# Kernel optimization log

Measured on AMD Instinct MI355X. Metric: run time of the kernel, lower is better.

## Reference

```python
import jax, jax.numpy as jnp
import numpy as np
import math

TOTAL_HEADS = 16
CONTEXTUAL_HEADS = 4


def _compute_slopes(heads):
    def slopes_power_of_2(n):
        start = 2 ** (-2 ** (-(math.log2(n) - 3)))
        ratio = start
        return [start * ratio ** i for i in range(n)]
    if math.log2(heads).is_integer():
        return slopes_power_of_2(heads)
    closest = 2 ** math.floor(math.log2(heads))
    return slopes_power_of_2(closest) + slopes_power_of_2(2 * closest)[0::2][: heads - closest]


def setup_inputs() -> dict:
    key = jax.random.key(0)
    kq, kk = jax.random.split(key)
    b, h, s, d = 1, 16, 2048, 64
    q = jax.random.normal(kq, (b, h, s, d), dtype=jnp.float32)
    k = jax.random.normal(kk, (b, h, s, d), dtype=jnp.float32)
    cross_attn_bias = jnp.zeros((TOTAL_HEADS, 1, 1), dtype=jnp.float32)
    return {"q": q, "k": k, "cross_attn_bias": cross_attn_bias,
            "i": s, "j": s, "offset": 0, "prefix": 16}


def reference(q, k, cross_attn_bias, i, j, offset, prefix):
    b = q.shape[0]
    ch = CONTEXTUAL_HEADS
    slopes = jnp.asarray(_compute_slopes(TOTAL_HEADS), dtype=jnp.float32).reshape(-1, 1, 1)  # [H,1,1]

    # base distance bias: -|j - i|, shape [i, j]
    i_arange = jnp.arange(offset, i + offset)
    j_arange = jnp.arange(j)
    bias = -jnp.abs(j_arange[None, :] - i_arange[:, None]).astype(jnp.float32)

    # contextual heads: data-dependent bias with bidirectional cumsum
    qc = q[:, :ch]
    kc = k[:, :ch]
    dots = jnp.einsum('bhid,bhjd->bhij', qc, kc) * (qc.shape[-1] ** -0.5)
    c_bias = -jax.nn.sigmoid(dots)  # [b, ch, i, j]
    upper = jnp.triu(jnp.ones((i, j), dtype=bool), offset + 1)
    lower = jnp.tril(jnp.ones((i, j), dtype=bool), offset - 1)
    c_up = jnp.cumsum(jnp.where(upper, c_bias, 0.0), axis=-1)
    c_lo = jnp.flip(jnp.cumsum(jnp.flip(jnp.where(lower, c_bias, 0.0), axis=-1), axis=-1), axis=-1)
    c_pos = c_up + c_lo  # [b, ch, i, j]

    bias_full = jnp.concatenate(
        [c_pos, jnp.broadcast_to(bias, (b, TOTAL_HEADS - ch, i, j))], axis=1)  # [b, H, i, j]

    attn_bias = slopes * bias_full  # symmetric path

    # prefix cross-attention bias
    is_prefix = jnp.arange(j) < prefix
    is_cross = (is_prefix[:, None] ^ is_prefix[None, :])[offset:]  # [i, j]
    attn_bias = jnp.where(is_cross, cross_attn_bias, attn_bias)
    return attn_bias
```

## Files before the change

kernel.cpp:

```cpp
#include <hip/hip_runtime.h>
#include <hip/hip_bf16.h>

typedef __bf16 bf16_t;
typedef bf16_t bf16x8 __attribute__((ext_vector_type(8)));
typedef float f32x4 __attribute__((ext_vector_type(4)));

#define TH 16
#define CH 4
#define DD 64
#define SJ 2048
#define SP (SJ + 4)
#define CTXB (SJ/16)
#define NCTX (CH*CTXB)
#define AROWS 32
#define NALIBI ((TH-CH)*(SJ/AROWS))
#define NBLK (NCTX + NALIBI)
#define WSK_BYTES ((size_t)CH*CTXB*2*64*16)

__device__ __forceinline__ float sigmoidf_(float x) {
    return __builtin_amdgcn_rcpf(1.0f + __expf(-x));
}

__device__ __forceinline__ float bsel(unsigned long long u, int e) {
    return __uint_as_float((((unsigned int)(u >> (16 * e)) & 0xffffu) << 16));
}

__global__ __launch_bounds__(256) void prep_kernel(
    const float* __restrict__ k, bf16_t* __restrict__ wsk)
{
    const int t    = (int)blockIdx.x * 256 + (int)threadIdx.x;
    const int h    = t >> 14;
    const int ct   = (t >> 7) & 127;
    const int kk   = (t >> 6) & 1;
    const int lane = t & 63;
    const int col  = ct * 16 + (lane & 15);
    const int db   = kk * 32 + (lane >> 4) * 8;
    const float* p = k + ((size_t)h * SJ + col) * DD + db;
    f32x4 v0 = *(const f32x4*)p;
    f32x4 v1 = *(const f32x4*)(p + 4);
    bf16x8 o;
    #pragma unroll
    for (int e = 0; e < 4; ++e) { o[e] = (bf16_t)v0[e]; o[e + 4] = (bf16_t)v1[e]; }
    *(bf16x8*)(wsk + (size_t)t * 8) = o;
}

__global__ __launch_bounds__(512, 4) void fused_kernel(
    const float* __restrict__ q, const float* __restrict__ k,
    const bf16_t* __restrict__ wsk, int use_ws,
    const float* __restrict__ cab, const int* __restrict__ offp,
    const int* __restrict__ prep, float* __restrict__ out)
{
    __shared__ bf16_t Smb[16][SP];
    __shared__ float tot[16][8];
    __shared__ float pd_in[16], pd_ex[16];
    const int tid  = (int)threadIdx.x;
    const int lane = tid & 63;
    const int w    = tid >> 6;
    const int offset = offp[0];
    const int prefix = prep[0];
    const int bx = (int)blockIdx.x;
    const int m5 = bx % 5;

    if (m5 < 2) {
        const int id = (bx / 5) * 2 + m5;
        const int h  = id >> 7;
        const int r0 = (id & (CTXB - 1)) << 4;
        const float* qh = q + (size_t)h * SJ * DD;
        const float* kh = k + (size_t)h * SJ * DD;

        bf16x8 afrag[2];
        {
            const int row   = r0 + (lane & 15);
            const int dbase = (lane >> 4) * 8;
            const float* qp = qh + (size_t)row * DD + dbase;
            #pragma unroll
            for (int kk = 0; kk < 2; ++kk) {
                f32x4 v0 = *(const f32x4*)(qp + kk * 32);
                f32x4 v1 = *(const f32x4*)(qp + kk * 32 + 4);
                #pragma unroll
                for (int e = 0; e < 4; ++e) {
                    afrag[kk][e]     = (bf16_t)v0[e];
                    afrag[kk][e + 4] = (bf16_t)v1[e];
                }
            }
        }
        if (tid < 16) { pd_in[tid] = 0.f; pd_ex[tid] = 0.f; }
        for (int t = 0; t < 16; ++t) {
            const int c0 = w * 256 + t * 16;
            f32x4 acc = {0.f, 0.f, 0.f, 0.f};
            if (use_ws) {
                const size_t fb = (((size_t)h * CTXB + (c0 >> 4)) * 2) * 64 + lane;
                #pragma unroll
                for (int kk = 0; kk < 2; ++kk) {
                    bf16x8 bfrag = *(const bf16x8*)(wsk + (fb + (size_t)kk * 64) * 8);
                    acc = __builtin_amdgcn_mfma_f32_16x16x32_bf16(afrag[kk], bfrag, acc, 0, 0, 0);
                }
            } else {
                #pragma unroll
                for (int kk = 0; kk < 2; ++kk) {
                    const int col = c0 + (lane & 15);
                    const int db  = kk * 32 + (lane >> 4) * 8;
                    const float* p = kh + (size_t)col * DD + db;
                    f32x4 v0 = *(const f32x4*)(p);
                    f32x4 v1 = *(const f32x4*)(p + 4);
                    bf16x8 bfrag;
                    #pragma unroll
                    for (int e = 0; e < 4; ++e) {
                        bfrag[e]     = (bf16_t)v0[e];
                        bfrag[e + 4] = (bf16_t)v1[e];
                    }
                    acc = __builtin_amdgcn_mfma_f32_16x16x32_bf16(afrag[kk], bfrag, acc, 0, 0, 0);
                }
            }
            const int ccol = c0 + (lane & 15);
            const int rb   = (lane >> 4) * 4;
            #pragma unroll
            for (int m = 0; m < 4; ++m)
                Smb[rb + m][ccol] = (bf16_t)sigmoidf_(acc[m] * 0.125f);
        }
        __syncthreads();

        const float slope = exp2f(-0.5f * (float)(h + 1));
        const float cabv  = cab[h];
        const int cb = w * 256 + lane * 4;
        float Pv[16][4], bse[16];
        #pragma unroll
        for (int rl = 0; rl < 16; ++rl) {
            const unsigned long long u = *(const unsigned long long*)(&Smb[rl][cb]);
            const float i0 = bsel(u, 0);
            const float i1 = i0 + bsel(u, 1);
            const float i2 = i1 + bsel(u, 2);
            const float i3 = i2 + bsel(u, 3);
            float x = i3;
            #pragma unroll
            for (int d = 1; d < 64; d <<= 1) {
                float y = __shfl_up(x, d);
                if (lane >= d) x += y;
            }
            if (lane == 63) tot[rl][w] = x;
            bse[rl]  = x - i3;
            Pv[rl][0] = i0; Pv[rl][1] = i1; Pv[rl][2] = i2; Pv[rl][3] = i3;
        }
        __syncthreads();
        #pragma unroll
        for (int rl = 0; rl < 16; ++rl) {
            float base = 0.f;
            #pragma unroll
            for (int s = 0; s < 7; ++s)
                base += (s < w) ? tot[rl][s] : 0.f;
            base += bse[rl];
            bse[rl] = base;
            #pragma unroll
            for (int e = 0; e < 4; ++e) Pv[rl][e] += base;
            const int rg = r0 + rl, dg = rg + offset;
            const int cin = dg < SJ ? dg : SJ - 1;
            const int cex = (dg - 1) < SJ ? dg - 1 : SJ - 1;
            #pragma unroll
            for (int e = 0; e < 4; ++e) {
                if (dg >= 0 && cin == cb + e) pd_in[rl] = Pv[rl][e];
                if (dg >= 1 && cex == cb + e) pd_ex[rl] = Pv[rl][e];
            }
        }
        __syncthreads();
        #pragma unroll
        for (int rl = 0; rl < 16; ++rl) {
            const int rg = r0 + rl, dg = rg + offset;
            const float pdin = pd_in[rl];
            const float pdex = pd_ex[rl];
            const bool rpre = dg < prefix;
            float* orow = out + ((size_t)h * SJ + rg) * (size_t)SJ;
            f32x4 o;
            #pragma unroll
            for (int e = 0; e < 4; ++e) {
                const int c  = cb + e;
                const float Pc = Pv[rl][e];
                const float Pm = e ? Pv[rl][e - 1] : bse[rl];
                const float cpos = (c > dg) ? -(Pc - pdin)
                                 : (c < dg) ? -(pdex - Pm) : 0.f;
                const bool cross = (c < prefix) != rpre;
                o[e] = cross ? cabv : slope * cpos;
            }
            *(f32x4*)(orow + cb) = o;
        }
    } else {
        const int id = (bx / 5) * 3 + (m5 - 2);
        const int h  = CH + (id >> 6);
        const int r0 = (id & 63) * AROWS;
        const float slope = exp2f(-0.5f * (float)(h + 1));
        const float cabv  = cab[h];
        #pragma unroll
        for (int rr = 0; rr < 4; ++rr) {
            const int rg = r0 + rr * 8 + w;
            const int dg = rg + offset;
            const bool rpre = dg < prefix;
            float* orow = out + ((size_t)h * SJ + rg) * (size_t)SJ;
            #pragma unroll
            for (int s = 0; s < 8; ++s) {
                const int cb = s * 256 + lane * 4;
                f32x4 o;
                #pragma unroll
                for (int e = 0; e < 4; ++e) {
                    const int c = cb + e;
                    const float v = -fabsf((float)(c - dg)) * slope;
                    const bool cross = (c < prefix) != rpre;
                    o[e] = cross ? cabv : v;
                }
                *(f32x4*)(orow + cb) = o;
            }
        }
    }
}

extern "C" void kernel_launch(void* const* d_in, const int* in_sizes, int n_in,
                              void* d_out, int out_size, void* d_ws, size_t ws_size,
                              hipStream_t stream) {
    const float* q    = (const float*)d_in[0];
    const float* k    = (const float*)d_in[1];
    const float* cab  = (const float*)d_in[2];
    const int*   offp = (const int*)d_in[5];
    const int*   prep = (const int*)d_in[6];
    float* out = (float*)d_out;
    bf16_t* wsk = (bf16_t*)d_ws;

    const int use_ws = (ws_size >= WSK_BYTES) ? 1 : 0;
    if (use_ws)
        prep_kernel<<<dim3(256), dim3(256), 0, stream>>>(k, wsk);
    fused_kernel<<<dim3(NBLK), dim3(512), 0, stream>>>(q, k, wsk, use_ws,
                                                       cab, offp, prep, out);
}
```

Before: 62.86 us.

## Remap blocks across XCDs, enlarge ALiBi row tiles, and cut scan register use

Block indices are now decoded XCD-aware (bx&7 picks the XCD, and even and odd slots alternate contextual and ALiBi work), replacing the mod-5 interleave. Each ALiBi block now writes 48 rows, which may cross head boundaries, so per-row head, slope and bias are computed inside the loop. The contextual scan stops holding the 64-float Pv array and keeps the packed bf16 words plus a base value, rebuilding prefix sums when needed. The aim is to balance work across XCDs and lower register pressure for occupancy, at the cost of extra recomputation and a different block count and balance.

```diff
diff --git a/kernel.cpp b/kernel.cpp
--- a/kernel.cpp
+++ b/kernel.cpp
@@ -12,8 +12,8 @@
 #define SP (SJ + 4)
 #define CTXB (SJ/16)
 #define NCTX (CH*CTXB)
-#define AROWS 32
-#define NALIBI ((TH-CH)*(SJ/AROWS))
+#define AROWS 48
+#define NALIBI ((TH-CH)*SJ/AROWS)
 #define NBLK (NCTX + NALIBI)
 #define WSK_BYTES ((size_t)CH*CTXB*2*64*16)
 
@@ -58,11 +58,12 @@
     const int w    = tid >> 6;
     const int offset = offp[0];
     const int prefix = prep[0];
-    const int bx = (int)blockIdx.x;
-    const int m5 = bx % 5;
-
-    if (m5 < 2) {
-        const int id = (bx / 5) * 2 + m5;
+    const int bx   = (int)blockIdx.x;
+    const int xcd  = bx & 7;
+    const int slot = bx >> 3;
+
+    if ((slot & 1) == 0) {
+        const int id = xcd * 64 + (slot >> 1);
         const int h  = id >> 7;
         const int r0 = (id & (CTXB - 1)) << 4;
         const float* qh = q + (size_t)h * SJ * DD;
@@ -123,14 +124,13 @@
         const float slope = exp2f(-0.5f * (float)(h + 1));
         const float cabv  = cab[h];
         const int cb = w * 256 + lane * 4;
-        float Pv[16][4], bse[16];
+        unsigned long long u[16];
+        float base_[16];
         #pragma unroll
         for (int rl = 0; rl < 16; ++rl) {
-            const unsigned long long u = *(const unsigned long long*)(&Smb[rl][cb]);
-            const float i0 = bsel(u, 0);
-            const float i1 = i0 + bsel(u, 1);
-            const float i2 = i1 + bsel(u, 2);
-            const float i3 = i2 + bsel(u, 3);
+            u[rl] = *(const unsigned long long*)(&Smb[rl][cb]);
+            const float i3 = ((bsel(u[rl], 0) + bsel(u[rl], 1))
+                            + (bsel(u[rl], 2) + bsel(u[rl], 3)));
             float x = i3;
             #pragma unroll
             for (int d = 1; d < 64; d <<= 1) {
@@ -138,27 +138,34 @@
                 if (lane >= d) x += y;
             }
             if (lane == 63) tot[rl][w] = x;
-            bse[rl]  = x - i3;
-            Pv[rl][0] = i0; Pv[rl][1] = i1; Pv[rl][2] = i2; Pv[rl][3] = i3;
+            base_[rl] = x - i3;
         }
         __syncthreads();
         #pragma unroll
         for (int rl = 0; rl < 16; ++rl) {
-            float base = 0.f;
+            float b = 0.f;
             #pragma unroll
             for (int s = 0; s < 7; ++s)
-                base += (s < w) ? tot[rl][s] : 0.f;
-            base += bse[rl];
-            bse[rl] = base;
-            #pragma unroll
-            for (int e = 0; e < 4; ++e) Pv[rl][e] += base;
+                b += (s < w) ? tot[rl][s] : 0.f;
+            base_[rl] += b;
             const int rg = r0 + rl, dg = rg + offset;
             const int cin = dg < SJ ? dg : SJ - 1;
             const int cex = (dg - 1) < SJ ? dg - 1 : SJ - 1;
-            #pragma unroll
-            for (int e = 0; e < 4; ++e) {
-                if (dg >= 0 && cin == cb + e) pd_in[rl] = Pv[rl][e];
-                if (dg >= 1 && cex == cb + e) pd_ex[rl] = Pv[rl][e];
+            if (dg >= 0 && (unsigned)(cin - cb) < 4u) {
+                const int e = cin - cb;
+                float pi = bsel(u[rl], 0);
+                if (e > 0) pi += bsel(u[rl], 1);
+                if (e > 1) pi += bsel(u[rl], 2);
+                if (e > 2) pi += bsel(u[rl], 3);
+                pd_in[rl] = base_[rl] + pi;
+            }
+            if (dg >= 1 && (unsigned)(cex - cb) < 4u) {
+                const int e = cex - cb;
+                float pi = bsel(u[rl], 0);
+                if (e > 0) pi += bsel(u[rl], 1);
+                if (e > 1) pi += bsel(u[rl], 2);
+                if (e > 2) pi += bsel(u[rl], 3);
+                pd_ex[rl] = base_[rl] + pi;
             }
         }
         __syncthreads();
@@ -168,32 +175,38 @@
             const float pdin = pd_in[rl];
             const float pdex = pd_ex[rl];
             const bool rpre = dg < prefix;
+            const float b  = base_[rl];
+            const float i0 = b  + bsel(u[rl], 0);
+            const float i1 = i0 + bsel(u[rl], 1);
+            const float i2 = i1 + bsel(u[rl], 2);
+            const float i3 = i2 + bsel(u[rl], 3);
+            const float Pc[4] = {i0, i1, i2, i3};
+            const float Pm[4] = {b, i0, i1, i2};
             float* orow = out + ((size_t)h * SJ + rg) * (size_t)SJ;
             f32x4 o;
             #pragma unroll
             for (int e = 0; e < 4; ++e) {
-                const int c  = cb + e;
-                const float Pc = Pv[rl][e];
-                const float Pm = e ? Pv[rl][e - 1] : bse[rl];
-                const float cpos = (c > dg) ? -(Pc - pdin)
-                                 : (c < dg) ? -(pdex - Pm) : 0.f;
+                const int c = cb + e;
+                const float cpos = (c > dg) ? -(Pc[e] - pdin)
+                                 : (c < dg) ? -(pdex - Pm[e]) : 0.f;
                 const bool cross = (c < prefix) != rpre;
                 o[e] = cross ? cabv : slope * cpos;
             }
             *(f32x4*)(orow + cb) = o;
         }
     } else {
-        const int id = (bx / 5) * 3 + (m5 - 2);
-        const int h  = CH + (id >> 6);
-        const int r0 = (id & 63) * AROWS;
-        const float slope = exp2f(-0.5f * (float)(h + 1));
-        const float cabv  = cab[h];
-        #pragma unroll
-        for (int rr = 0; rr < 4; ++rr) {
-            const int rg = r0 + rr * 8 + w;
-            const int dg = rg + offset;
+        const int aid = xcd * 64 + (slot >> 1);
+        const int R0  = aid * AROWS;
+        #pragma unroll
+        for (int rr = 0; rr < 6; ++rr) {
+            const int R  = R0 + rr * 8 + w;
+            const int h  = CH + (R >> 11);
+            const int r  = R & (SJ - 1);
+            const int dg = r + offset;
+            const float slope = exp2f(-0.5f * (float)(h + 1));
+            const float cabv  = cab[h];
             const bool rpre = dg < prefix;
-            float* orow = out + ((size_t)h * SJ + rg) * (size_t)SJ;
+            float* orow = out + ((size_t)h * SJ + r) * (size_t)SJ;
             #pragma unroll
             for (int s = 0; s < 8; ++s) {
                 const int cb = s * 256 + lane * 4;
```

Result: slower. 73.09 us (+16.3%).

## Halve block size and rows per contextual block, recompute prefix sums from packed bf16

Applied to the files above, without the earlier changes.

Blocks shrink from 512 to 256 threads, and each contextual block now covers 8 rows instead of 16, so there are twice as many blocks with less shared memory each. Each wave handles two 256-column segments. The per-row prefix values are no longer kept in registers; the packed bf16 words are held and the prefix is rebuilt at output time, which lowers register pressure. The costs are that half of each MFMA output tile is wasted (rows are duplicated via lane&7) and the K fragments are reloaded for every 8 rows, doubling that read traffic.

```diff
diff --git a/kernel.cpp b/kernel.cpp
--- a/kernel.cpp
+++ b/kernel.cpp
@@ -4,24 +4,25 @@
 typedef __bf16 bf16_t;
 typedef bf16_t bf16x8 __attribute__((ext_vector_type(8)));
 typedef float f32x4 __attribute__((ext_vector_type(4)));
+typedef unsigned long long u64_t;
 
 #define TH 16
 #define CH 4
 #define DD 64
 #define SJ 2048
 #define SP (SJ + 4)
-#define CTXB (SJ/16)
-#define NCTX (CH*CTXB)
-#define AROWS 32
-#define NALIBI ((TH-CH)*(SJ/AROWS))
+#define RROWS 8
+#define NCTX (CH*SJ/RROWS)
+#define AROWS 16
+#define NALIBI ((TH-CH)*SJ/AROWS)
 #define NBLK (NCTX + NALIBI)
-#define WSK_BYTES ((size_t)CH*CTXB*2*64*16)
+#define WSK_BYTES ((size_t)CH*(SJ/16)*2*64*16)
 
 __device__ __forceinline__ float sigmoidf_(float x) {
     return __builtin_amdgcn_rcpf(1.0f + __expf(-x));
 }
 
-__device__ __forceinline__ float bsel(unsigned long long u, int e) {
+__device__ __forceinline__ float bsel(u64_t u, int e) {
     return __uint_as_float((((unsigned int)(u >> (16 * e)) & 0xffffu) << 16));
 }
 
@@ -44,15 +45,15 @@
     *(bf16x8*)(wsk + (size_t)t * 8) = o;
 }
 
-__global__ __launch_bounds__(512, 4) void fused_kernel(
+__global__ __launch_bounds__(256, 4) void fused_kernel(
     const float* __restrict__ q, const float* __restrict__ k,
     const bf16_t* __restrict__ wsk, int use_ws,
     const float* __restrict__ cab, const int* __restrict__ offp,
     const int* __restrict__ prep, float* __restrict__ out)
 {
-    __shared__ bf16_t Smb[16][SP];
-    __shared__ float tot[16][8];
-    __shared__ float pd_in[16], pd_ex[16];
+    __shared__ bf16_t Smb[RROWS][SP];
+    __shared__ float tot[RROWS][8];
+    __shared__ float pd_in[RROWS], pd_ex[RROWS];
     const int tid  = (int)threadIdx.x;
     const int lane = tid & 63;
     const int w    = tid >> 6;
@@ -63,14 +64,14 @@
 
     if (m5 < 2) {
         const int id = (bx / 5) * 2 + m5;
-        const int h  = id >> 7;
-        const int r0 = (id & (CTXB - 1)) << 4;
+        const int h  = id >> 8;
+        const int r0 = (id & 255) * RROWS;
         const float* qh = q + (size_t)h * SJ * DD;
         const float* kh = k + (size_t)h * SJ * DD;
 
         bf16x8 afrag[2];
         {
-            const int row   = r0 + (lane & 15);
+            const int row   = r0 + ((lane & 15) & 7);
             const int dbase = (lane >> 4) * 8;
             const float* qp = qh + (size_t)row * DD + dbase;
             #pragma unroll
@@ -84,12 +85,13 @@
                 }
             }
         }
-        if (tid < 16) { pd_in[tid] = 0.f; pd_ex[tid] = 0.f; }
-        for (int t = 0; t < 16; ++t) {
-            const int c0 = w * 256 + t * 16;
+        if (tid < RROWS) { pd_in[tid] = 0.f; pd_ex[tid] = 0.f; }
+        const int rb = (lane >> 4) * 4;
+        for (int t = 0; t < 32; ++t) {
+            const int c0 = w * 512 + t * 16;
             f32x4 acc = {0.f, 0.f, 0.f, 0.f};
             if (use_ws) {
-                const size_t fb = (((size_t)h * CTXB + (c0 >> 4)) * 2) * 64 + lane;
+                const size_t fb = (((size_t)h * (SJ/16) + (c0 >> 4)) * 2) * 64 + lane;
                 #pragma unroll
                 for (int kk = 0; kk < 2; ++kk) {
                     bf16x8 bfrag = *(const bf16x8*)(wsk + (fb + (size_t)kk * 64) * 8);
@@ -112,85 +114,111 @@
                     acc = __builtin_amdgcn_mfma_f32_16x16x32_bf16(afrag[kk], bfrag, acc, 0, 0, 0);
                 }
             }
-            const int ccol = c0 + (lane & 15);
-            const int rb   = (lane >> 4) * 4;
-            #pragma unroll
-            for (int m = 0; m < 4; ++m)
-                Smb[rb + m][ccol] = (bf16_t)sigmoidf_(acc[m] * 0.125f);
+            if (rb < RROWS) {
+                const int ccol = c0 + (lane & 15);
+                #pragma unroll
+                for (int m = 0; m < 4; ++m)
+                    Smb[rb + m][ccol] = (bf16_t)sigmoidf_(acc[m] * 0.125f);
+            }
         }
         __syncthreads();
 
         const float slope = exp2f(-0.5f * (float)(h + 1));
         const float cabv  = cab[h];
-        const int cb = w * 256 + lane * 4;
-        float Pv[16][4], bse[16];
-        #pragma unroll
-        for (int rl = 0; rl < 16; ++rl) {
-            const unsigned long long u = *(const unsigned long long*)(&Smb[rl][cb]);
-            const float i0 = bsel(u, 0);
-            const float i1 = i0 + bsel(u, 1);
-            const float i2 = i1 + bsel(u, 2);
-            const float i3 = i2 + bsel(u, 3);
-            float x = i3;
-            #pragma unroll
-            for (int d = 1; d < 64; d <<= 1) {
-                float y = __shfl_up(x, d);
-                if (lane >= d) x += y;
-            }
-            if (lane == 63) tot[rl][w] = x;
-            bse[rl]  = x - i3;
-            Pv[rl][0] = i0; Pv[rl][1] = i1; Pv[rl][2] = i2; Pv[rl][3] = i3;
+        u64_t u[RROWS][2];
+        float base_[RROWS][2];
+        #pragma unroll
+        for (int rl = 0; rl < RROWS; ++rl) {
+            #pragma unroll
+            for (int g = 0; g < 2; ++g) {
+                const int cb = (w + g * 4) * 256 + lane * 4;
+                const u64_t uu = *(const u64_t*)(&Smb[rl][cb]);
+                u[rl][g] = uu;
+                const float i3 = (bsel(uu, 0) + bsel(uu, 1)) + (bsel(uu, 2) + bsel(uu, 3));
+                float x = i3;
+                #pragma unroll
+                for (int d = 1; d < 64; d <<= 1) {
+                    float y = __shfl_up(x, d);
+                    if (lane >= d) x += y;
+                }
+                if (lane == 63) tot[rl][w + g * 4] = x;
+                base_[rl][g] = x - i3;
+            }
         }
         __syncthreads();
         #pragma unroll
-        for (int rl = 0; rl < 16; ++rl) {
-            float base = 0.f;
-            #pragma unroll
-            for (int s = 0; s < 7; ++s)
-                base += (s < w) ? tot[rl][s] : 0.f;
-            base += bse[rl];
-            bse[rl] = base;
-            #pragma unroll
-            for (int e = 0; e < 4; ++e) Pv[rl][e] += base;
+        for (int rl = 0; rl < RROWS; ++rl) {
             const int rg = r0 + rl, dg = rg + offset;
             const int cin = dg < SJ ? dg : SJ - 1;
             const int cex = (dg - 1) < SJ ? dg - 1 : SJ - 1;
             #pragma unroll
-            for (int e = 0; e < 4; ++e) {
-                if (dg >= 0 && cin == cb + e) pd_in[rl] = Pv[rl][e];
-                if (dg >= 1 && cex == cb + e) pd_ex[rl] = Pv[rl][e];
+            for (int g = 0; g < 2; ++g) {
+                const int sb = w + g * 4;
+                const int cb = sb * 256 + lane * 4;
+                float b = 0.f;
+                #pragma unroll
+                for (int s = 0; s < 7; ++s)
+                    b += (s < sb) ? tot[rl][s] : 0.f;
+                base_[rl][g] += b;
+                const u64_t uu = u[rl][g];
+                if (dg >= 0 && (unsigned)(cin - cb) < 4u) {
+                    const int e = cin - cb;
+                    float pi = bsel(uu, 0);
+                    if (e > 0) pi += bsel(uu, 1);
+                    if (e > 1) pi += bsel(uu, 2);
+                    if (e > 2) pi += bsel(uu, 3);
+                    pd_in[rl] = base_[rl][g] + pi;
+                }
+                if (dg >= 1 && (unsigned)(cex - cb) < 4u) {
+                    const int e = cex - cb;
+                    float pi = bsel(uu, 0);
+                    if (e > 0) pi += bsel(uu, 1);
+                    if (e > 1) pi += bsel(uu, 2);
+                    if (e > 2) pi += bsel(uu, 3);
+                    pd_ex[rl] = base_[rl][g] + pi;
+                }
             }
         }
         __syncthreads();
         #pragma unroll
-        for (int rl = 0; rl < 16; ++rl) {
+        for (int rl = 0; rl < RROWS; ++rl) {
             const int rg = r0 + rl, dg = rg + offset;
             const float pdin = pd_in[rl];
             const float pdex = pd_ex[rl];
             const bool rpre = dg < prefix;
             float* orow = out + ((size_t)h * SJ + rg) * (size_t)SJ;
-            f32x4 o;
-            #pragma unroll
-            for (int e = 0; e < 4; ++e) {
-                const int c  = cb + e;
-                const float Pc = Pv[rl][e];
-                const float Pm = e ? Pv[rl][e - 1] : bse[rl];
-                const float cpos = (c > dg) ? -(Pc - pdin)
-                                 : (c < dg) ? -(pdex - Pm) : 0.f;
-                const bool cross = (c < prefix) != rpre;
-                o[e] = cross ? cabv : slope * cpos;
-            }
-            *(f32x4*)(orow + cb) = o;
+            #pragma unroll
+            for (int g = 0; g < 2; ++g) {
+                const int cb = (w + g * 4) * 256 + lane * 4;
+                const u64_t uu = u[rl][g];
+                const float b  = base_[rl][g];
+                const float i0 = b  + bsel(uu, 0);
+                const float i1 = i0 + bsel(uu, 1);
+                const float i2 = i1 + bsel(uu, 2);
+                const float i3 = i2 + bsel(uu, 3);
+                const float Pc[4] = {i0, i1, i2, i3};
+                const float Pm[4] = {b, i0, i1, i2};
+                f32x4 o;
+                #pragma unroll
+                for (int e = 0; e < 4; ++e) {
+                    const int c = cb + e;
+                    const float cpos = (c > dg) ? -(Pc[e] - pdin)
+                                     : (c < dg) ? -(pdex - Pm[e]) : 0.f;
+                    const bool cross = (c < prefix) != rpre;
+                    o[e] = cross ? cabv : slope * cpos;
+                }
+                *(f32x4*)(orow + cb) = o;
+            }
         }
     } else {
         const int id = (bx / 5) * 3 + (m5 - 2);
-        const int h  = CH + (id >> 6);
-        const int r0 = (id & 63) * AROWS;
+        const int h  = CH + (id >> 7);
+        const int r0 = (id & 127) * AROWS;
         const float slope = exp2f(-0.5f * (float)(h + 1));
         const float cabv  = cab[h];
         #pragma unroll
         for (int rr = 0; rr < 4; ++rr) {
-            const int rg = r0 + rr * 8 + w;
+            const int rg = r0 + w * 4 + rr;
             const int dg = rg + offset;
             const bool rpre = dg < prefix;
             float* orow = out + ((size_t)h * SJ + rg) * (size_t)SJ;
@@ -225,6 +253,6 @@
     const int use_ws = (ws_size >= WSK_BYTES) ? 1 : 0;
     if (use_ws)
         prep_kernel<<<dim3(256), dim3(256), 0, stream>>>(k, wsk);
-    fused_kernel<<<dim3(NBLK), dim3(512), 0, stream>>>(q, k, wsk, use_ws,
+    fused_kernel<<<dim3(NBLK), dim3(256), 0, stream>>>(q, k, wsk, use_ws,
                                                        cab, offp, prep, out);
 }
```

New measurement: 75.20 us. 19.6% more time.
